# Kernel tuning notes

Measured on AMD Instinct MI355X. Metric: run time of the kernel, lower is better.

The kernel has to match this reference:

```python
import jax, jax.numpy as jnp
import numpy as np

NUM_EMBEDDINGS = 1024
EMBEDDING_DIM = 64
COMMITMENT_COST = 0.25


def setup_inputs() -> dict:
    key = jax.random.key(0)
    k1, k2 = jax.random.split(key)
    z = jax.random.normal(k1, (16, EMBEDDING_DIM, 64, 64), dtype=jnp.float32)
    # nn.Embedding init: uniform(-1/K, 1/K)
    emb = jax.random.uniform(
        k2, (NUM_EMBEDDINGS, EMBEDDING_DIM), dtype=jnp.float32,
        minval=-1.0 / NUM_EMBEDDINGS, maxval=1.0 / NUM_EMBEDDINGS)
    return {"z": z, "emb": emb}


def reference(z, emb):
    # b c h w -> b h w c
    zc = jnp.transpose(z, (0, 2, 3, 1))
    B, H, W, D = zc.shape
    zf = zc.reshape(-1, D)  # [N, D]
    K = emb.shape[0]

    # L2 distances: ||z||^2 + ||e||^2 - 2 z e^T   -> [N, K]
    distances = (jnp.sum(zf * zf, axis=1, keepdims=True)
                 + jnp.sum(emb * emb, axis=1)
                 - 2.0 * jnp.matmul(zf, emb.T))
    encoding_indices = jnp.argmin(distances, axis=1)  # [N]

    # one_hot @ emb  ==  gather
    quantized = emb[encoding_indices].reshape(zc.shape)  # [B,H,W,D]

    reconstruction_errors = jnp.sum((quantized - zc) ** 2, axis=-1).reshape(-1)
    avg_error = jnp.mean(reconstruction_errors)

    e_latent_loss = jnp.mean((jax.lax.stop_gradient(quantized) - zc) ** 2)
    q_latent_loss = jnp.mean((quantized - jax.lax.stop_gradient(zc)) ** 2)
    loss = q_latent_loss + COMMITMENT_COST * e_latent_loss

    # straight-through estimator
    quantized_st = zc + jax.lax.stop_gradient(quantized - zc)
    out = jnp.transpose(quantized_st, (0, 3, 1, 2))  # b h w c -> b c h w

    # perplexity: avg one-hot usage (histogram instead of dense one-hot)
    N = zf.shape[0]
    counts = jnp.zeros((K,), dtype=jnp.float32).at[encoding_indices].add(1.0)
    avg_probs = counts / N
    perplexity = jnp.exp(-jnp.sum(avg_probs * jnp.log(avg_probs + 1e-10)))

    return out, loss, perplexity, avg_error
```

## Files before the change

### kernel.cpp

```cpp
#include <hip/hip_runtime.h>
#include <stdint.h>

#define HW   4096
#define NEMB 1024

typedef float        f32x4  __attribute__((ext_vector_type(4)));
typedef short        bf16x8 __attribute__((ext_vector_type(8)));
typedef unsigned int u32x4  __attribute__((ext_vector_type(4)));

#define CVTPK(D, LO, HI) asm("v_cvt_pk_bf16_f32 %0, %1, %2" : "=v"(D) : "v"(LO), "v"(HI))

__device__ __forceinline__ void gload_lds16(const float* g, float* l) {
    __builtin_amdgcn_global_load_lds(
        (const __attribute__((address_space(1))) void*)(uintptr_t)g,
        (__attribute__((address_space(3))) void*)(uintptr_t)l, 16, 0, 0);
}

__global__ __launch_bounds__(128) void vq_init(const float* __restrict__ emb,
                                               unsigned int* __restrict__ counts,
                                               float* __restrict__ errsum,
                                               float* __restrict__ ens) {
    const int k = blockIdx.x * 128 + threadIdx.x;
    counts[k] = 0u;
    if (k == 0) *errsum = 0.0f;
    const float* e = emb + k * 64;
    float a[8] = {0,0,0,0,0,0,0,0};
    #pragma unroll
    for (int c = 0; c < 16; ++c) {
        f32x4 v = *(const f32x4*)(e + c * 4);
        a[(4*c+0) & 7] += v.x * v.x;
        a[(4*c+1) & 7] += v.y * v.y;
        a[(4*c+2) & 7] += v.z * v.z;
        a[(4*c+3) & 7] += v.w * v.w;
    }
    ens[k] = 1.0f + (((a[0]+a[1]) + (a[2]+a[3])) + ((a[4]+a[5]) + (a[6]+a[7])));
}

__global__ __launch_bounds__(512, 4)
void vq_main(const float* __restrict__ z, const float* __restrict__ emb,
             const float* __restrict__ ens,
             float* __restrict__ out, unsigned int* __restrict__ counts,
             float* __restrict__ errsum)
{
    __shared__ __attribute__((aligned(16))) float z_lds[64 * 128];
    __shared__ __attribute__((aligned(16))) unsigned int et_w[256 * 32];
    __shared__ __attribute__((aligned(16))) float ens_lds[NEMB];
    __shared__ int   idx_sh[128];
    __shared__ float errp[512];

    const int t   = threadIdx.x;
    const int n0  = blockIdx.x * 128;
    const int bb  = n0 >> 12;
    const int hw0 = n0 & 4095;
    const float* zb = z + bb * (64 * HW) + hw0;

    #pragma unroll
    for (int it = 0; it < 4; ++it) {
        const int p = it * 512 + t;
        gload_lds16(zb + (p >> 5) * HW + (p & 31) * 4, z_lds + p * 4);
    }
    if (t < 256) gload_lds16(ens + t * 4, ens_lds + t * 4);

    #pragma unroll
    for (int it = 0; it < 4; ++it) {
        const int q = it * 512 + t;
        const int r = q >> 3, c = q & 7;
        const float* s2 = emb + r * 64 + c * 8;
        f32x4 e0 = *(const f32x4*)s2;
        f32x4 e1 = *(const f32x4*)(s2 + 4);
        u32x4 v;
        CVTPK(v.x, e0.x, e0.y); CVTPK(v.y, e0.z, e0.w);
        CVTPK(v.z, e1.x, e1.y); CVTPK(v.w, e1.z, e1.w);
        *(u32x4*)&et_w[r * 32 + ((c ^ (r & 7)) << 2)] = v;
    }
    __syncthreads();

    const int l   = t & 63;
    const int wv  = t >> 6;
    const int col = l & 15;
    const int bg  = l >> 4;

    bf16x8 a0, a1;
    {
        const int xs = wv * 16 + col;
        u32x4 wa, wb;
        #pragma unroll
        for (int p2 = 0; p2 < 4; ++p2) {
            float lo = z_lds[(bg * 8 + p2 * 2    ) * 128 + xs];
            float hi = z_lds[(bg * 8 + p2 * 2 + 1) * 128 + xs];
            CVTPK(wa[p2], lo, hi);
            float lo2 = z_lds[(32 + bg * 8 + p2 * 2    ) * 128 + xs];
            float hi2 = z_lds[(32 + bg * 8 + p2 * 2 + 1) * 128 + xs];
            CVTPK(wb[p2], lo2, hi2);
        }
        a0 = __builtin_bit_cast(bf16x8, wa);
        a1 = __builtin_bit_cast(bf16x8, wb);
    }

    const int slot0 = bg ^ (col & 7);
    const unsigned int* ep0 = et_w + col * 32 + slot0 * 4;
    const unsigned int* ep1 = et_w + col * 32 + (slot0 ^ 4) * 4;
    const float* ensp = ens_lds + col;

    unsigned int mkey[4] = {~0u, ~0u, ~0u, ~0u};

    #pragma unroll
    for (int kt = 0; kt < 4; ++kt) {
        f32x4 pf[8];
        if (kt < 3) {
            const float* src = emb + (kt + 1) * 256 * 64;
            #pragma unroll
            for (int it = 0; it < 4; ++it) {
                const int q = it * 512 + t;
                const float* s2 = src + (q >> 3) * 64 + (q & 7) * 8;
                pf[it * 2]     = *(const f32x4*)s2;
                pf[it * 2 + 1] = *(const f32x4*)(s2 + 4);
            }
        }

        #pragma unroll
        for (int i = 0; i < 16; ++i) {
            u32x4 bw0 = *(const u32x4*)(ep0 + i * 512);
            u32x4 bw1 = *(const u32x4*)(ep1 + i * 512);
            float en1 = ensp[kt * 256 + i * 16];
            f32x4 cc = {0.0f, 0.0f, 0.0f, 0.0f};
            cc = __builtin_amdgcn_mfma_f32_16x16x32_bf16(a0, __builtin_bit_cast(bf16x8, bw0), cc, 0, 0, 0);
            cc = __builtin_amdgcn_mfma_f32_16x16x32_bf16(a1, __builtin_bit_cast(bf16x8, bw1), cc, 0, 0, 0);
            const unsigned int kg = (unsigned int)(kt * 256 + i * 16 + col);
            #pragma unroll
            for (int j = 0; j < 4; ++j) {
                float s = fmaf(-2.0f, cc[j], en1);
                unsigned int key = (__builtin_bit_cast(unsigned int, s) & 0xFFFFFC00u) | kg;
                mkey[j] = mkey[j] < key ? mkey[j] : key;
            }
        }

        __syncthreads();
        if (kt < 3) {
            #pragma unroll
            for (int it = 0; it < 4; ++it) {
                const int q = it * 512 + t;
                const int r = q >> 3, c = q & 7;
                u32x4 v;
                CVTPK(v.x, pf[it*2].x,   pf[it*2].y);
                CVTPK(v.y, pf[it*2].z,   pf[it*2].w);
                CVTPK(v.z, pf[it*2+1].x, pf[it*2+1].y);
                CVTPK(v.w, pf[it*2+1].z, pf[it*2+1].w);
                *(u32x4*)&et_w[r * 32 + ((c ^ (r & 7)) << 2)] = v;
            }
            __syncthreads();
        }
    }

    #pragma unroll
    for (int j = 0; j < 4; ++j) {
        #pragma unroll
        for (int m = 1; m <= 8; m <<= 1) {
            unsigned int o = (unsigned int)__shfl_xor((int)mkey[j], m, 64);
            mkey[j] = mkey[j] < o ? mkey[j] : o;
        }
    }
    if (col == 0) {
        #pragma unroll
        for (int j = 0; j < 4; ++j)
            idx_sh[wv * 16 + bg * 4 + j] = (int)(mkey[j] & 1023u);
    }
    __syncthreads();

    if (t < 128) atomicAdd(&counts[idx_sh[t]], 1u);

    {
        const int x  = t & 127;
        const int cg = t >> 7;
        const int idx = idx_sh[x];
        const float* er = emb + idx * 64;
        float* ob = out + bb * (64 * HW) + hw0 + x;
        float part = 0.0f;
        #pragma unroll
        for (int cq = 0; cq < 4; ++cq) {
            const int c = cg * 16 + cq * 4;
            f32x4 e4 = *(const f32x4*)&er[c];
            float z0 = z_lds[(c+0) * 128 + x];
            float z1 = z_lds[(c+1) * 128 + x];
            float z2 = z_lds[(c+2) * 128 + x];
            float z3 = z_lds[(c+3) * 128 + x];
            ob[(c+0) * HW] = z0 + (e4.x - z0);
            ob[(c+1) * HW] = z1 + (e4.y - z1);
            ob[(c+2) * HW] = z2 + (e4.z - z2);
            ob[(c+3) * HW] = z3 + (e4.w - z3);
            float d0 = z0 - e4.x, d1 = z1 - e4.y, d2 = z2 - e4.z, d3 = z3 - e4.w;
            part = fmaf(d0, d0, part); part = fmaf(d1, d1, part);
            part = fmaf(d2, d2, part); part = fmaf(d3, d3, part);
        }
        errp[t] = part;
    }
    __syncthreads();
    if (t < 128) {
        float s = (errp[t] + errp[t + 128]) + (errp[t + 256] + errp[t + 384]);
        #pragma unroll
        for (int off = 32; off >= 1; off >>= 1) s += __shfl_down(s, off, 64);
        if ((t & 63) == 0) atomicAdd(errsum, s);
    }
}

__global__ __launch_bounds__(256) void vq_fin(const unsigned int* __restrict__ counts,
                                              const float* __restrict__ errsum,
                                              float* __restrict__ scal)
{
    __shared__ float part[4];
    const int t = threadIdx.x;
    float s = 0.0f;
    for (int k = t; k < NEMB; k += 256) {
        float p = (float)counts[k] * (1.0f / 65536.0f);
        s += p * logf(p + 1e-10f);
    }
    #pragma unroll
    for (int off = 32; off >= 1; off >>= 1) s += __shfl_down(s, off, 64);
    if ((t & 63) == 0) part[t >> 6] = s;
    __syncthreads();
    if (t == 0) {
        float tot = (part[0] + part[1]) + (part[2] + part[3]);
        float es  = *errsum;
        scal[0] = 1.25f * (es * (1.0f / 4194304.0f));
        scal[1] = expf(-tot);
        scal[2] = es * (1.0f / 65536.0f);
    }
}

extern "C" void kernel_launch(void* const* d_in, const int* in_sizes, int n_in,
                              void* d_out, int out_size, void* d_ws, size_t ws_size,
                              hipStream_t stream) {
    const float* z   = (const float*)d_in[0];
    const float* emb = (const float*)d_in[1];
    float* out = (float*)d_out;
    unsigned int* counts = (unsigned int*)d_ws;
    float* errsum = (float*)((char*)d_ws + 4096);
    float* ens    = (float*)((char*)d_ws + 8192);

    vq_init<<<8, 128, 0, stream>>>(emb, counts, errsum, ens);
    vq_main<<<512, 512, 0, stream>>>(z, emb, ens, out, counts, errsum);
    vq_fin<<<1, 256, 0, stream>>>(counts, errsum, out + 4194304);
}
```

Measured before the change: 42.91 us.

## Precompute swizzled fp16 codebook once and stream it into LDS via direct loads

The init kernel now converts the codebook to packed fp16 in the swizzled LDS layout and writes it to workspace. Each main block then copies codebook tiles with global-to-LDS DMA loads, where before every block loaded fp32 rows into registers, converted them and wrote them to LDS. The MFMA changes from bf16 to fp16 inputs, and the packed-key argmin becomes an exact float compare with index tie-break. This removes redundant per-block conversion work and register prefetch pressure, but the tile prefetch is no longer overlapped with compute and fp16 adds overflow/precision risk.

```diff
diff --git a/kernel.cpp b/kernel.cpp
--- a/kernel.cpp
+++ b/kernel.cpp
@@ -5,10 +5,10 @@
 #define NEMB 1024
 
 typedef float        f32x4  __attribute__((ext_vector_type(4)));
-typedef short        bf16x8 __attribute__((ext_vector_type(8)));
+typedef short        h16x8  __attribute__((ext_vector_type(8)));
 typedef unsigned int u32x4  __attribute__((ext_vector_type(4)));
 
-#define CVTPK(D, LO, HI) asm("v_cvt_pk_bf16_f32 %0, %1, %2" : "=v"(D) : "v"(LO), "v"(HI))
+#define CVTPKH(D, LO, HI) asm("v_cvt_pkrtz_f16_f32 %0, %1, %2" : "=v"(D) : "v"(LO), "v"(HI))
 
 __device__ __forceinline__ void gload_lds16(const float* g, float* l) {
     __builtin_amdgcn_global_load_lds(
@@ -19,26 +19,33 @@
 __global__ __launch_bounds__(128) void vq_init(const float* __restrict__ emb,
                                                unsigned int* __restrict__ counts,
                                                float* __restrict__ errsum,
-                                               float* __restrict__ ens) {
+                                               float* __restrict__ ens,
+                                               unsigned int* __restrict__ embw) {
     const int k = blockIdx.x * 128 + threadIdx.x;
     counts[k] = 0u;
     if (k == 0) *errsum = 0.0f;
     const float* e = emb + k * 64;
     float a[8] = {0,0,0,0,0,0,0,0};
-    #pragma unroll
-    for (int c = 0; c < 16; ++c) {
-        f32x4 v = *(const f32x4*)(e + c * 4);
-        a[(4*c+0) & 7] += v.x * v.x;
-        a[(4*c+1) & 7] += v.y * v.y;
-        a[(4*c+2) & 7] += v.z * v.z;
-        a[(4*c+3) & 7] += v.w * v.w;
-    }
-    ens[k] = 1.0f + (((a[0]+a[1]) + (a[2]+a[3])) + ((a[4]+a[5]) + (a[6]+a[7])));
+    unsigned int* dst = embw + k * 32;
+    #pragma unroll
+    for (int c = 0; c < 8; ++c) {
+        f32x4 v0 = *(const f32x4*)(e + c * 8);
+        f32x4 v1 = *(const f32x4*)(e + c * 8 + 4);
+        a[0] += v0.x * v0.x; a[1] += v0.y * v0.y;
+        a[2] += v0.z * v0.z; a[3] += v0.w * v0.w;
+        a[4] += v1.x * v1.x; a[5] += v1.y * v1.y;
+        a[6] += v1.z * v1.z; a[7] += v1.w * v1.w;
+        u32x4 w;
+        CVTPKH(w.x, v0.x, v0.y); CVTPKH(w.y, v0.z, v0.w);
+        CVTPKH(w.z, v1.x, v1.y); CVTPKH(w.w, v1.z, v1.w);
+        *(u32x4*)&dst[(c ^ (k & 7)) << 2] = w;
+    }
+    ens[k] = ((a[0]+a[1]) + (a[2]+a[3])) + ((a[4]+a[5]) + (a[6]+a[7]));
 }
 
 __global__ __launch_bounds__(512, 4)
 void vq_main(const float* __restrict__ z, const float* __restrict__ emb,
-             const float* __restrict__ ens,
+             const float* __restrict__ ens, const unsigned int* __restrict__ embw,
              float* __restrict__ out, unsigned int* __restrict__ counts,
              float* __restrict__ errsum)
 {
@@ -60,18 +67,10 @@
         gload_lds16(zb + (p >> 5) * HW + (p & 31) * 4, z_lds + p * 4);
     }
     if (t < 256) gload_lds16(ens + t * 4, ens_lds + t * 4);
-
     #pragma unroll
     for (int it = 0; it < 4; ++it) {
-        const int q = it * 512 + t;
-        const int r = q >> 3, c = q & 7;
-        const float* s2 = emb + r * 64 + c * 8;
-        f32x4 e0 = *(const f32x4*)s2;
-        f32x4 e1 = *(const f32x4*)(s2 + 4);
-        u32x4 v;
-        CVTPK(v.x, e0.x, e0.y); CVTPK(v.y, e0.z, e0.w);
-        CVTPK(v.z, e1.x, e1.y); CVTPK(v.w, e1.z, e1.w);
-        *(u32x4*)&et_w[r * 32 + ((c ^ (r & 7)) << 2)] = v;
+        const int p = it * 512 + t;
+        gload_lds16((const float*)embw + p * 4, (float*)et_w + p * 4);
     }
     __syncthreads();
 
@@ -80,7 +79,7 @@
     const int col = l & 15;
     const int bg  = l >> 4;
 
-    bf16x8 a0, a1;
+    h16x8 a0, a1;
     {
         const int xs = wv * 16 + col;
         u32x4 wa, wb;
@@ -88,13 +87,13 @@
         for (int p2 = 0; p2 < 4; ++p2) {
             float lo = z_lds[(bg * 8 + p2 * 2    ) * 128 + xs];
             float hi = z_lds[(bg * 8 + p2 * 2 + 1) * 128 + xs];
-            CVTPK(wa[p2], lo, hi);
+            CVTPKH(wa[p2], lo, hi);
             float lo2 = z_lds[(32 + bg * 8 + p2 * 2    ) * 128 + xs];
             float hi2 = z_lds[(32 + bg * 8 + p2 * 2 + 1) * 128 + xs];
-            CVTPK(wb[p2], lo2, hi2);
-        }
-        a0 = __builtin_bit_cast(bf16x8, wa);
-        a1 = __builtin_bit_cast(bf16x8, wb);
+            CVTPKH(wb[p2], lo2, hi2);
+        }
+        a0 = __builtin_bit_cast(h16x8, wa);
+        a1 = __builtin_bit_cast(h16x8, wb);
     }
 
     const int slot0 = bg ^ (col & 7);
@@ -102,51 +101,34 @@
     const unsigned int* ep1 = et_w + col * 32 + (slot0 ^ 4) * 4;
     const float* ensp = ens_lds + col;
 
-    unsigned int mkey[4] = {~0u, ~0u, ~0u, ~0u};
+    float mval[4] = {__builtin_inff(), __builtin_inff(), __builtin_inff(), __builtin_inff()};
+    int   midx[4] = {0, 0, 0, 0};
 
     #pragma unroll
     for (int kt = 0; kt < 4; ++kt) {
-        f32x4 pf[8];
-        if (kt < 3) {
-            const float* src = emb + (kt + 1) * 256 * 64;
-            #pragma unroll
-            for (int it = 0; it < 4; ++it) {
-                const int q = it * 512 + t;
-                const float* s2 = src + (q >> 3) * 64 + (q & 7) * 8;
-                pf[it * 2]     = *(const f32x4*)s2;
-                pf[it * 2 + 1] = *(const f32x4*)(s2 + 4);
-            }
-        }
-
         #pragma unroll
         for (int i = 0; i < 16; ++i) {
             u32x4 bw0 = *(const u32x4*)(ep0 + i * 512);
             u32x4 bw1 = *(const u32x4*)(ep1 + i * 512);
-            float en1 = ensp[kt * 256 + i * 16];
+            float en = ensp[kt * 256 + i * 16];
             f32x4 cc = {0.0f, 0.0f, 0.0f, 0.0f};
-            cc = __builtin_amdgcn_mfma_f32_16x16x32_bf16(a0, __builtin_bit_cast(bf16x8, bw0), cc, 0, 0, 0);
-            cc = __builtin_amdgcn_mfma_f32_16x16x32_bf16(a1, __builtin_bit_cast(bf16x8, bw1), cc, 0, 0, 0);
-            const unsigned int kg = (unsigned int)(kt * 256 + i * 16 + col);
+            cc = __builtin_amdgcn_mfma_f32_16x16x32_f16(a0, __builtin_bit_cast(h16x8, bw0), cc, 0, 0, 0);
+            cc = __builtin_amdgcn_mfma_f32_16x16x32_f16(a1, __builtin_bit_cast(h16x8, bw1), cc, 0, 0, 0);
+            const int kg = kt * 256 + i * 16 + col;
             #pragma unroll
             for (int j = 0; j < 4; ++j) {
-                float s = fmaf(-2.0f, cc[j], en1);
-                unsigned int key = (__builtin_bit_cast(unsigned int, s) & 0xFFFFFC00u) | kg;
-                mkey[j] = mkey[j] < key ? mkey[j] : key;
+                const float s = fmaf(-2.0f, cc[j], en);
+                if (s < mval[j]) { mval[j] = s; midx[j] = kg; }
             }
         }
 
         __syncthreads();
         if (kt < 3) {
+            const float* src = (const float*)(embw + (kt + 1) * 8192);
             #pragma unroll
             for (int it = 0; it < 4; ++it) {
-                const int q = it * 512 + t;
-                const int r = q >> 3, c = q & 7;
-                u32x4 v;
-                CVTPK(v.x, pf[it*2].x,   pf[it*2].y);
-                CVTPK(v.y, pf[it*2].z,   pf[it*2].w);
-                CVTPK(v.z, pf[it*2+1].x, pf[it*2+1].y);
-                CVTPK(v.w, pf[it*2+1].z, pf[it*2+1].w);
-                *(u32x4*)&et_w[r * 32 + ((c ^ (r & 7)) << 2)] = v;
+                const int p = it * 512 + t;
+                gload_lds16(src + p * 4, (float*)et_w + p * 4);
             }
             __syncthreads();
         }
@@ -154,16 +136,14 @@
 
     #pragma unroll
     for (int j = 0; j < 4; ++j) {
-        #pragma unroll
-        for (int m = 1; m <= 8; m <<= 1) {
-            unsigned int o = (unsigned int)__shfl_xor((int)mkey[j], m, 64);
-            mkey[j] = mkey[j] < o ? mkey[j] : o;
-        }
-    }
-    if (col == 0) {
-        #pragma unroll
-        for (int j = 0; j < 4; ++j)
-            idx_sh[wv * 16 + bg * 4 + j] = (int)(mkey[j] & 1023u);
+        float m = mval[j]; int id = midx[j];
+        #pragma unroll
+        for (int mk = 1; mk <= 8; mk <<= 1) {
+            float m2 = __shfl_xor(m, mk, 64);
+            int   i2 = __shfl_xor(id, mk, 64);
+            if (m2 < m || (m2 == m && i2 < id)) { m = m2; id = i2; }
+        }
+        if (col == 0) idx_sh[wv * 16 + bg * 4 + j] = id;
     }
     __syncthreads();
 
@@ -236,8 +216,9 @@
     unsigned int* counts = (unsigned int*)d_ws;
     float* errsum = (float*)((char*)d_ws + 4096);
     float* ens    = (float*)((char*)d_ws + 8192);
-
-    vq_init<<<8, 128, 0, stream>>>(emb, counts, errsum, ens);
-    vq_main<<<512, 512, 0, stream>>>(z, emb, ens, out, counts, errsum);
+    unsigned int* embw = (unsigned int*)((char*)d_ws + 16384);
+
+    vq_init<<<8, 128, 0, stream>>>(emb, counts, errsum, ens, embw);
+    vq_main<<<512, 512, 0, stream>>>(z, emb, ens, embw, out, counts, errsum);
     vq_fin<<<1, 256, 0, stream>>>(counts, errsum, out + 4194304);
 }
```

New measurement: 46.95 us. +9.4%, slower.

## Fuse codebook norm computation into main kernel, replace init kernel with memset

Applied to the files above, without the earlier changes.

Removes the separate vq_init kernel. Each block now computes the squared norms of each 256-entry codebook tile from the fp32 values it already loads for bf16 conversion, using a wave-shuffle reduction, and stores them in a smaller LDS array. Counts and errsum are zeroed with hipMemsetAsync instead. This drops one kernel launch and its global round-trip, at the cost of redundant norm arithmetic and shuffles in every block, plus a memset node.

```diff
diff --git a/kernel.cpp b/kernel.cpp
--- a/kernel.cpp
+++ b/kernel.cpp
@@ -16,35 +16,14 @@
         (__attribute__((address_space(3))) void*)(uintptr_t)l, 16, 0, 0);
 }
 
-__global__ __launch_bounds__(128) void vq_init(const float* __restrict__ emb,
-                                               unsigned int* __restrict__ counts,
-                                               float* __restrict__ errsum,
-                                               float* __restrict__ ens) {
-    const int k = blockIdx.x * 128 + threadIdx.x;
-    counts[k] = 0u;
-    if (k == 0) *errsum = 0.0f;
-    const float* e = emb + k * 64;
-    float a[8] = {0,0,0,0,0,0,0,0};
-    #pragma unroll
-    for (int c = 0; c < 16; ++c) {
-        f32x4 v = *(const f32x4*)(e + c * 4);
-        a[(4*c+0) & 7] += v.x * v.x;
-        a[(4*c+1) & 7] += v.y * v.y;
-        a[(4*c+2) & 7] += v.z * v.z;
-        a[(4*c+3) & 7] += v.w * v.w;
-    }
-    ens[k] = 1.0f + (((a[0]+a[1]) + (a[2]+a[3])) + ((a[4]+a[5]) + (a[6]+a[7])));
-}
-
 __global__ __launch_bounds__(512, 4)
 void vq_main(const float* __restrict__ z, const float* __restrict__ emb,
-             const float* __restrict__ ens,
              float* __restrict__ out, unsigned int* __restrict__ counts,
              float* __restrict__ errsum)
 {
     __shared__ __attribute__((aligned(16))) float z_lds[64 * 128];
     __shared__ __attribute__((aligned(16))) unsigned int et_w[256 * 32];
-    __shared__ __attribute__((aligned(16))) float ens_lds[NEMB];
+    __shared__ __attribute__((aligned(16))) float ens_lds[256];
     __shared__ int   idx_sh[128];
     __shared__ float errp[512];
 
@@ -59,7 +38,6 @@
         const int p = it * 512 + t;
         gload_lds16(zb + (p >> 5) * HW + (p & 31) * 4, z_lds + p * 4);
     }
-    if (t < 256) gload_lds16(ens + t * 4, ens_lds + t * 4);
 
     #pragma unroll
     for (int it = 0; it < 4; ++it) {
@@ -72,6 +50,12 @@
         CVTPK(v.x, e0.x, e0.y); CVTPK(v.y, e0.z, e0.w);
         CVTPK(v.z, e1.x, e1.y); CVTPK(v.w, e1.z, e1.w);
         *(u32x4*)&et_w[r * 32 + ((c ^ (r & 7)) << 2)] = v;
+        float pn = (e0.x*e0.x + e0.y*e0.y) + (e0.z*e0.z + e0.w*e0.w)
+                 + (e1.x*e1.x + e1.y*e1.y) + (e1.z*e1.z + e1.w*e1.w);
+        pn += __shfl_xor(pn, 1, 64);
+        pn += __shfl_xor(pn, 2, 64);
+        pn += __shfl_xor(pn, 4, 64);
+        if (c == 0) ens_lds[r] = 1.0f + pn;
     }
     __syncthreads();
 
@@ -122,7 +106,7 @@
         for (int i = 0; i < 16; ++i) {
             u32x4 bw0 = *(const u32x4*)(ep0 + i * 512);
             u32x4 bw1 = *(const u32x4*)(ep1 + i * 512);
-            float en1 = ensp[kt * 256 + i * 16];
+            float en1 = ensp[i * 16];
             f32x4 cc = {0.0f, 0.0f, 0.0f, 0.0f};
             cc = __builtin_amdgcn_mfma_f32_16x16x32_bf16(a0, __builtin_bit_cast(bf16x8, bw0), cc, 0, 0, 0);
             cc = __builtin_amdgcn_mfma_f32_16x16x32_bf16(a1, __builtin_bit_cast(bf16x8, bw1), cc, 0, 0, 0);
@@ -147,6 +131,14 @@
                 CVTPK(v.z, pf[it*2+1].x, pf[it*2+1].y);
                 CVTPK(v.w, pf[it*2+1].z, pf[it*2+1].w);
                 *(u32x4*)&et_w[r * 32 + ((c ^ (r & 7)) << 2)] = v;
+                float pn = (pf[it*2].x*pf[it*2].x + pf[it*2].y*pf[it*2].y)
+                         + (pf[it*2].z*pf[it*2].z + pf[it*2].w*pf[it*2].w)
+                         + (pf[it*2+1].x*pf[it*2+1].x + pf[it*2+1].y*pf[it*2+1].y)
+                         + (pf[it*2+1].z*pf[it*2+1].z + pf[it*2+1].w*pf[it*2+1].w);
+                pn += __shfl_xor(pn, 1, 64);
+                pn += __shfl_xor(pn, 2, 64);
+                pn += __shfl_xor(pn, 4, 64);
+                if (c == 0) ens_lds[r] = 1.0f + pn;
             }
             __syncthreads();
         }
@@ -235,9 +227,8 @@
     float* out = (float*)d_out;
     unsigned int* counts = (unsigned int*)d_ws;
     float* errsum = (float*)((char*)d_ws + 4096);
-    float* ens    = (float*)((char*)d_ws + 8192);
-
-    vq_init<<<8, 128, 0, stream>>>(emb, counts, errsum, ens);
-    vq_main<<<512, 512, 0, stream>>>(z, emb, ens, out, counts, errsum);
+
+    hipMemsetAsync(d_ws, 0, 8192, stream);
+    vq_main<<<512, 512, 0, stream>>>(z, emb, out, counts, errsum);
     vq_fin<<<1, 256, 0, stream>>>(counts, errsum, out + 4194304);
 }
```

Result: slower. 44.82 us (+4.5%).
